# Optimization experiments

Measured on AMD Instinct MI355X. Metric: run time of the kernel, lower is better.

The kernel has to match this reference:

```python
import jax, jax.numpy as jnp
import numpy as np

N_QUBITS = 10
N_LAYERS = 4
DIM = 2 ** N_QUBITS


def _bit(v, q, n):
    return (v >> (n - 1 - q)) & 1


def _cnot_indices(control, target, n):
    idx0, idx1 = [], []
    for i in range(2 ** n):
        if _bit(i, control, n) == 1 and _bit(i, target, n) == 0:
            idx0.append(i)
            idx1.append(i | (1 << (n - 1 - target)))
    return np.asarray(idx0, np.int32), np.asarray(idx1, np.int32)


# static precomputed CNOT swap indices for pairs (q, (q+1) % n)
_CNOT = [_cnot_indices(q, (q + 1) % N_QUBITS, N_QUBITS) for q in range(N_QUBITS)]
# Z expectation masks: [n_qubits, dim] of +/-1
_ZMASK = np.array([[1.0 - 2.0 * _bit(i, q, N_QUBITS) for i in range(DIM)]
                   for q in range(N_QUBITS)], np.float32)


def _rx(t):
    c = jnp.cos(t / 2.0).astype(jnp.complex64)
    s = jnp.sin(t / 2.0).astype(jnp.complex64)
    return jnp.stack([jnp.stack([c, -1j * s], -1),
                      jnp.stack([-1j * s, c], -1)], -2)


def _ry(t):
    c = jnp.cos(t / 2.0).astype(jnp.complex64)
    s = jnp.sin(t / 2.0).astype(jnp.complex64)
    return jnp.stack([jnp.stack([c, -s], -1),
                      jnp.stack([s, c], -1)], -2)


def _rz(t):
    tc = t.astype(jnp.complex64)
    e0 = jnp.exp(-1j * tc / 2.0)
    e1 = jnp.exp(1j * tc / 2.0)
    z = jnp.zeros_like(e0)
    return jnp.stack([jnp.stack([e0, z], -1),
                      jnp.stack([z, e1], -1)], -2)


def _apply_gate(state, gate, q):
    # state: [b, DIM] complex64; gate: [2,2] or [b,2,2]
    b = state.shape[0]
    psi = state.reshape((b,) + (2,) * N_QUBITS)
    psi = jnp.moveaxis(psi, q + 1, N_QUBITS).reshape(b, DIM // 2, 2)
    if gate.ndim == 3:
        out = jnp.einsum('bmi,bij->bmj', psi, gate)
    else:
        out = jnp.einsum('bmi,ij->bmj', psi, gate)
    out = out.reshape((b,) + (2,) * N_QUBITS)
    out = jnp.moveaxis(out, N_QUBITS, q + 1)
    return out.reshape(b, DIM)


def _cnot(state, idx0, idx1):
    return state.at[:, idx0].set(state[:, idx1]).at[:, idx1].set(state[:, idx0])


def setup_inputs() -> dict:
    key = jax.random.key(0)
    k1, k2, k3, k4 = jax.random.split(key, 4)
    x = jax.random.normal(k1, (16384, 3), jnp.float32)
    enc_W = jax.random.normal(k2, (N_QUBITS, 3), jnp.float32) * 0.3
    enc_b = jax.random.normal(k3, (N_QUBITS,), jnp.float32) * 0.1
    theta = jax.random.normal(k4, (N_LAYERS, N_QUBITS, 3), jnp.float32) * 0.04
    return {"x": x, "enc_W": enc_W, "enc_b": enc_b, "theta": theta}


def reference(x, enc_W, enc_b, theta):
    b = x.shape[0]
    enc = jnp.pi * jnp.tanh(x @ enc_W.T + enc_b)  # [b, n_qubits]
    state = jnp.zeros((b, DIM), jnp.complex64).at[:, 0].set(1.0 + 0j)
    # batched encoding RY rotations
    for q in range(N_QUBITS):
        state = _apply_gate(state, _ry(enc[:, q]), q)
    # variational layers (shared gate across batch)
    for layer in range(N_LAYERS):
        for q in range(N_QUBITS):
            state = _apply_gate(state, _rx(theta[layer, q, 0]), q)
            state = _apply_gate(state, _ry(theta[layer, q, 1]), q)
            state = _apply_gate(state, _rz(theta[layer, q, 2]), q)
        for idx0, idx1 in _CNOT:
            state = _cnot(state, idx0, idx1)
    probs = jnp.square(state.real) + jnp.square(state.imag)  # [b, DIM]
    return probs @ jnp.asarray(_ZMASK).T  # [b, n_qubits]
```

## Files before the change

kernel.cpp:

```cpp
#include <hip/hip_runtime.h>
#include <stdint.h>

#define NQ 10
#define NL 4

typedef unsigned int u32;
typedef _Float16 f16x8 __attribute__((ext_vector_type(8)));
typedef float f32x16 __attribute__((ext_vector_type(16)));
typedef u32 u32x4 __attribute__((ext_vector_type(4)));

constexpr u32 FRc(u32 r) {
    u32 r0 = r & 1, r1 = (r >> 1) & 1, r2 = (r >> 2) & 1, r3 = (r >> 3) & 1, r4 = (r >> 4) & 1;
    return (r4 << 9) | ((r3 ^ r4) << 8) | ((r2 ^ r3) << 7) | ((r1 ^ r2) << 6) |
           ((r0 ^ r1) << 5) | (r0 << 4);
}
constexpr u32 FCc(u32 c) {
    u32 c0 = c & 1, c1 = (c >> 1) & 1, c2 = (c >> 2) & 1, c3 = (c >> 3) & 1, c4 = (c >> 4) & 1;
    return (c0 << 9) | (c0 << 8) | (c4 << 4) | ((c3 ^ c4) << 3) | ((c2 ^ c3) << 2) |
           ((c1 ^ c2) << 1) | (c0 ^ c1);
}

__device__ __forceinline__ f32x16 mfma16(f16x8 a, f16x8 b, f32x16 c) {
    return __builtin_amdgcn_mfma_f32_32x32x16_f16(a, b, c, 0, 0, 0);
}
__device__ __forceinline__ f32x16 zero16() {
    f32x16 z;
#pragma unroll
    for (int i = 0; i < 16; i++) z[i] = 0.f;
    return z;
}
__device__ __forceinline__ f16x8 negf(f16x8 v) {
    u32x4 u = __builtin_bit_cast(u32x4, v);
#pragma unroll
    for (int i = 0; i < 4; i++) u[i] ^= 0x80008000u;
    return __builtin_bit_cast(f16x8, u);
}
__device__ __forceinline__ u32 pk2(float a, float b) {
    auto h = __builtin_amdgcn_cvt_pkrtz(a, b);
    return __builtin_bit_cast(u32, h);
}
__device__ __forceinline__ u32 permlo(u32 a, u32 b) { return __builtin_amdgcn_perm(b, a, 0x05040100u); }
__device__ __forceinline__ u32 permhi(u32 a, u32 b) { return __builtin_amdgcn_perm(b, a, 0x07060302u); }
__device__ __forceinline__ f16x8 mk8(u32 a, u32 b, u32 c, u32 d) {
    u32x4 v; v[0] = a; v[1] = b; v[2] = c; v[3] = d;
    return __builtin_bit_cast(f16x8, v);
}
template <int MASK>
__device__ __forceinline__ float swz(float v) {
    return __int_as_float(__builtin_amdgcn_ds_swizzle(__float_as_int(v), (MASK << 10) | 0x1F));
}
__device__ __forceinline__ u32 bpermu(int addr, u32 v) {
    return (u32)__builtin_amdgcn_ds_bpermute(addr, (int)v);
}
__device__ __forceinline__ void cmulh(float ar, float ai, float br, float bi, float& cr, float& ci) {
    cr = ar * br - ai * bi;
    ci = ar * bi + ai * br;
}

__device__ __forceinline__ void c2a(const f32x16& V, bool hb, int addr32, u32 (&o)[8]) {
    u32 pw[8];
#pragma unroll
    for (int p = 0; p < 8; p++) pw[p] = pk2(V[2 * p], V[2 * p + 1]);
    u32 s0 = hb ? pw[0] : pw[2];
    u32 s1 = hb ? pw[1] : pw[3];
    u32 s2 = hb ? pw[4] : pw[6];
    u32 s3 = hb ? pw[5] : pw[7];
    u32 r0 = bpermu(addr32, s0), r1 = bpermu(addr32, s1);
    u32 r2 = bpermu(addr32, s2), r3 = bpermu(addr32, s3);
    o[0] = hb ? r0 : pw[0]; o[1] = hb ? r1 : pw[1];
    o[2] = hb ? pw[2] : r0; o[3] = hb ? pw[3] : r1;
    o[4] = hb ? r2 : pw[4]; o[5] = hb ? r3 : pw[5];
    o[6] = hb ? pw[6] : r2; o[7] = hb ? pw[7] : r3;
}

__global__ void tq_prep(const float* __restrict__ theta, uint16_t* __restrict__ frag) {
    __shared__ float g[NL * NQ][8];
    int tt = threadIdx.x;
    if (tt < NL * NQ) {
        float hx = 0.5f * theta[tt * 3 + 0];
        float hy = 0.5f * theta[tt * 3 + 1];
        float hz = 0.5f * theta[tt * 3 + 2];
        float cx = cosf(hx), sx = sinf(hx);
        float cy = cosf(hy), sy = sinf(hy);
        float cz = cosf(hz), sz = sinf(hz);
        float m00r = cx * cy, m00i = -sx * sy;
        float m01r = -cx * sy, m01i = -sx * cy;
        float m10r = cx * sy, m10i = -sx * cy;
        float m11r = cx * cy, m11i = sx * sy;
        float g00r, g00i, g01r, g01i, g10r, g10i, g11r, g11i;
        cmulh(m00r, m00i, cz, -sz, g00r, g00i);
        cmulh(m10r, m10i, cz, -sz, g10r, g10i);
        cmulh(m01r, m01i, cz, sz, g01r, g01i);
        cmulh(m11r, m11i, cz, sz, g11r, g11i);
        g[tt][0] = g00r; g[tt][1] = g00i; g[tt][2] = g01r; g[tt][3] = g01i;
        g[tt][4] = g10r; g[tt][5] = g10i; g[tt][6] = g11r; g[tt][7] = g11i;
    }
    __syncthreads();
    int t = blockIdx.x * blockDim.x + tt;
    int lane = t & 63, kh = (t >> 6) & 1, part = (t >> 7) & 1, mat = (t >> 8) & 1, l = t >> 9;
    int mn = lane & 31, hf = (lane >> 5) & 1;
#pragma unroll
    for (int j = 0; j < 8; j++) {
        int k = kh * 16 + hf * 8 + j;
        float pr = 1.f, pi = 0.f;
#pragma unroll
        for (int u = 0; u < 5; u++) {
            int q = mat ? (5 + u) : u;
            int bi_ = (k >> (4 - u)) & 1;
            int bo_ = (mn >> (4 - u)) & 1;
            const float* gg = g[l * NQ + q];
            float er = gg[(bi_ * 2 + bo_) * 2 + 0];
            float ei = gg[(bi_ * 2 + bo_) * 2 + 1];
            float nr, ni;
            cmulh(pr, pi, er, ei, nr, ni);
            pr = nr;
            pi = ni;
        }
        float v = part ? pi : pr;
        _Float16 h = (_Float16)v;
        frag[t * 8 + j] = __builtin_bit_cast(unsigned short, h);
    }
    if (blockIdx.x == 0 && tt < 128) {
        int ln = tt & 63, kh2 = tt >> 6;
        int q = ln & 31, hf2 = (ln >> 5) & 1;
        u32 M = (q == 0) ? 0xFu : (q == 1) ? 0x18u : (q == 2) ? 0x1Cu : (q == 3) ? 0x1Eu : 0x1Fu;
        uint16_t* o = frag + ((32 + kh2) * 64 + ln) * 8;
#pragma unroll
        for (int j = 0; j < 8; j++) {
            int k = kh2 * 16 + hf2 * 8 + j;
            float v = (__builtin_popcount((u32)k & M) & 1) ? -1.f : 1.f;
            _Float16 h = (_Float16)v;
            o[j] = __builtin_bit_cast(unsigned short, h);
        }
    }
}

__global__ __launch_bounds__(256) void tq_main(
    const float* __restrict__ x, const float* __restrict__ encW,
    const float* __restrict__ encb, const uint16_t* __restrict__ frag,
    float* __restrict__ out, int batch) {
    __shared__ u32 smem[4 * 1024];
    int tid = threadIdx.x;
    int wave = (blockIdx.x * blockDim.x + tid) >> 6;
    int lane = tid & 63;
    if (wave >= batch) return;
    u32* slab = smem + (tid >> 6) * 1024;
    const int col = lane & 31;
    const int half_ = lane >> 5;
    const bool hb = half_ != 0;
    const int addr32 = (lane ^ 32) << 2;
    const u32 Fc5 = FCc((u32)col);

    float x0 = x[wave * 3 + 0], x1 = x[wave * 3 + 1], x2 = x[wave * 3 + 2];
    float hc = 1.f, hs = 0.f;
    if (lane < NQ) {
        float tta = 3.14159265358979323846f *
                    tanhf(x0 * encW[lane * 3 + 0] + x1 * encW[lane * 3 + 1] +
                          x2 * encW[lane * 3 + 2] + encb[lane]);
        float h = 0.5f * tta;
        hc = cosf(h);
        hs = sinf(h);
    }
    float fcv[NQ], fsv[NQ];
#pragma unroll
    for (int q = 0; q < NQ; q++) {
        fcv[q] = __shfl(hc, q, 64);
        fsv[q] = __shfl(hs, q, 64);
    }
    float colf = 1.f;
    colf *= ((col >> 4) & 1) ? -fsv[5] : fcv[5];
    colf *= ((col >> 3) & 1) ? -fsv[6] : fcv[6];
    colf *= ((col >> 2) & 1) ? -fsv[7] : fcv[7];
    colf *= ((col >> 1) & 1) ? -fsv[8] : fcv[8];
    colf *= (col & 1) ? -fsv[9] : fcv[9];
    float f1h = half_ ? -fsv[1] : fcv[1];
    float gj[8];
#pragma unroll
    for (int j = 0; j < 8; j++) {
        gj[j] = ((j & 4) ? -fsv[2] : fcv[2]) * ((j & 2) ? -fsv[3] : fcv[3]) *
                ((j & 1) ? -fsv[4] : fcv[4]);
    }
    f16x8 Sr0, Sr1, Si0, Si1;
#pragma unroll
    for (int j = 0; j < 8; j++) {
        Sr0[j] = (_Float16)(fcv[0] * f1h * gj[j] * colf);
        Sr1[j] = (_Float16)(-fsv[0] * f1h * gj[j] * colf);
        Si0[j] = (_Float16)0.f;
        Si1[j] = (_Float16)0.f;
    }

    const f16x8* fr = (const f16x8*)frag;
#define FRAG(f) fr[((f)*64) + lane]

    f32x16 Ur, Ui;
#pragma unroll
    for (int l = 0; l < NL; l++) {
        f16x8 Wr0 = FRAG(8 * l + 0), Wr1 = FRAG(8 * l + 1);
        f16x8 Wi0 = FRAG(8 * l + 2), Wi1 = FRAG(8 * l + 3);
        f16x8 Vr0 = FRAG(8 * l + 4), Vr1 = FRAG(8 * l + 5);
        f16x8 Vi0 = FRAG(8 * l + 6), Vi1 = FRAG(8 * l + 7);

        f32x16 Tr = zero16(), Ti = zero16();
        Tr = mfma16(Sr0, Wr0, Tr);
        Tr = mfma16(Sr1, Wr1, Tr);
        Ti = mfma16(Sr0, Wi0, Ti);
        Ti = mfma16(Sr1, Wi1, Ti);
        if (l > 0) {
            f16x8 nSi0 = negf(Si0), nSi1 = negf(Si1);
            Tr = mfma16(nSi0, Wi0, Tr);
            Tr = mfma16(nSi1, Wi1, Tr);
            Ti = mfma16(Si0, Wr0, Ti);
            Ti = mfma16(Si1, Wr1, Ti);
        }

        u32 oR[8], oI[8];
        c2a(Tr, hb, addr32, oR);
        c2a(Ti, hb, addr32, oI);
        f16x8 TAr0 = mk8(oR[0], oR[1], oR[2], oR[3]);
        f16x8 TAr1 = mk8(oR[4], oR[5], oR[6], oR[7]);
        f16x8 TAi0 = mk8(oI[0], oI[1], oI[2], oI[3]);
        f16x8 TAi1 = mk8(oI[4], oI[5], oI[6], oI[7]);

        Ur = zero16();
        Ui = zero16();
        Ur = mfma16(TAr0, Vr0, Ur);
        Ur = mfma16(TAr1, Vr1, Ur);
        {
            f16x8 nTAi0 = negf(TAi0), nTAi1 = negf(TAi1);
            Ur = mfma16(nTAi0, Vi0, Ur);
            Ur = mfma16(nTAi1, Vi1, Ur);
        }
        Ui = mfma16(TAr0, Vi0, Ui);
        Ui = mfma16(TAr1, Vi1, Ui);
        Ui = mfma16(TAi0, Vr0, Ui);
        Ui = mfma16(TAi1, Vr1, Ui);

        if (l < NL - 1) {
            {
                u32* wb = slab + col + half_ * (4 * 32);
#pragma unroll
                for (int gi = 0; gi < 16; gi++) {
                    int rb = (gi & 3) + 8 * (gi >> 2);
                    wb[rb * 32] = pk2(Ur[gi], Ui[gi]);
                }
            }
            u32 sb[16];
            {
                u32 fh = Fc5 ^ (half_ ? FRc(8) : 0u);
#pragma unroll
                for (int kh = 0; kh < 2; kh++)
#pragma unroll
                    for (int j = 0; j < 8; j++)
                        sb[kh * 8 + j] = slab[FRc(kh * 16 + j) ^ fh];
            }
            Sr0 = mk8(permlo(sb[0], sb[1]), permlo(sb[2], sb[3]),
                      permlo(sb[4], sb[5]), permlo(sb[6], sb[7]));
            Sr1 = mk8(permlo(sb[8], sb[9]), permlo(sb[10], sb[11]),
                      permlo(sb[12], sb[13]), permlo(sb[14], sb[15]));
            Si0 = mk8(permhi(sb[0], sb[1]), permhi(sb[2], sb[3]),
                      permhi(sb[4], sb[5]), permhi(sb[6], sb[7]));
            Si1 = mk8(permhi(sb[8], sb[9]), permhi(sb[10], sb[11]),
                      permhi(sb[12], sb[13]), permhi(sb[14], sb[15]));
        }
    }

    f32x16 P;
#pragma unroll
    for (int gi = 0; gi < 16; gi++) P[gi] = Ur[gi] * Ur[gi] + Ui[gi] * Ui[gi];
    u32 po[8];
    c2a(P, hb, addr32, po);
    f16x8 PB0 = mk8(po[0], po[1], po[2], po[3]);
    f16x8 PB1 = mk8(po[4], po[5], po[6], po[7]);
    f16x8 Srw0 = FRAG(32), Srw1 = FRAG(33);
    f32x16 D = mfma16(Srw0, PB0, mfma16(Srw1, PB1, zero16()));

    u32 b4 = (col >> 4) & 1, b3 = (col >> 3) & 1, b2 = (col >> 2) & 1,
        b1 = (col >> 1) & 1, b0 = col & 1;
    u32 p4 = b4, p43 = p4 ^ b3, p432 = p43 ^ b2, p4321 = p432 ^ b1, pall = p4321 ^ b0;
    u32 sg[6];
    sg[0] = hb ? 0u : pall;
    sg[1] = hb ? p4 : 0u;
    sg[2] = hb ? p43 : 0u;
    sg[3] = hb ? p432 : 0u;
    sg[4] = hb ? 0u : p4321;
    sg[5] = hb ? 0u : pall;
    float red[6];
#pragma unroll
    for (int s = 0; s < 6; s++) {
        float v = __uint_as_float(__float_as_uint(D[s]) ^ (sg[s] << 31));
        v += swz<1>(v);
        v += swz<2>(v);
        v += swz<4>(v);
        v += swz<8>(v);
        v += swz<16>(v);
        red[s] = v;
    }
    int cc = col - ((col >= 4) ? 4 : 0);
    float v = red[0];
    v = (cc == 1) ? red[1] : v;
    v = (cc == 2) ? red[2] : v;
    v = (cc == 3) ? red[3] : v;
    v = (cc == 4) ? red[4] : v;
    v = (cc == 5) ? red[5] : v;
    bool st = hb ? (col >= 4 && col < 8) : (col < 4 || col == 8 || col == 9);
    if (st) out[wave * NQ + col] = v;
}

extern "C" void kernel_launch(void* const* d_in, const int* in_sizes, int n_in,
                              void* d_out, int out_size, void* d_ws, size_t ws_size,
                              hipStream_t stream) {
    const float* x = (const float*)d_in[0];
    const float* encW = (const float*)d_in[1];
    const float* encb = (const float*)d_in[2];
    const float* th = (const float*)d_in[3];
    float* out = (float*)d_out;
    uint16_t* frag = (uint16_t*)d_ws;
    int batch = in_sizes[0] / 3;

    tq_prep<<<2, 1024, 0, stream>>>(th, frag);
    int total_threads = batch * 64;
    tq_main<<<(total_threads + 255) / 256, 256, 0, stream>>>(x, encW, encb, frag, out, batch);
}
```

Before: 102.6 us.

## Replace LDS transpose between layers with cross-lane swizzle and bpermute

Removes the per-wave shared-memory slab used to re-layout the state between variational layers. The accumulator is now rearranged in registers with ds_swizzle and ds_bpermute. The permutation is folded into the precomputed gate fragments by Gray-coding the output index for the non-final layers. It also replaces __shfl broadcasts with readlane. This removes LDS write/read traffic and the LDS allocation per block, at the cost of more VALU selects and cross-lane ops.

```diff
diff --git a/kernel.cpp b/kernel.cpp
--- a/kernel.cpp
+++ b/kernel.cpp
@@ -9,16 +9,6 @@
 typedef float f32x16 __attribute__((ext_vector_type(16)));
 typedef u32 u32x4 __attribute__((ext_vector_type(4)));
 
-constexpr u32 FRc(u32 r) {
-    u32 r0 = r & 1, r1 = (r >> 1) & 1, r2 = (r >> 2) & 1, r3 = (r >> 3) & 1, r4 = (r >> 4) & 1;
-    return (r4 << 9) | ((r3 ^ r4) << 8) | ((r2 ^ r3) << 7) | ((r1 ^ r2) << 6) |
-           ((r0 ^ r1) << 5) | (r0 << 4);
-}
-constexpr u32 FCc(u32 c) {
-    u32 c0 = c & 1, c1 = (c >> 1) & 1, c2 = (c >> 2) & 1, c3 = (c >> 3) & 1, c4 = (c >> 4) & 1;
-    return (c0 << 9) | (c0 << 8) | (c4 << 4) | ((c3 ^ c4) << 3) | ((c2 ^ c3) << 2) |
-           ((c1 ^ c2) << 1) | (c0 ^ c1);
-}
 
 __device__ __forceinline__ f32x16 mfma16(f16x8 a, f16x8 b, f32x16 c) {
     return __builtin_amdgcn_mfma_f32_32x32x16_f16(a, b, c, 0, 0, 0);
@@ -49,8 +39,15 @@
 __device__ __forceinline__ float swz(float v) {
     return __int_as_float(__builtin_amdgcn_ds_swizzle(__float_as_int(v), (MASK << 10) | 0x1F));
 }
+template <int MASK>
+__device__ __forceinline__ u32 swzu(u32 v) {
+    return (u32)__builtin_amdgcn_ds_swizzle((int)v, (MASK << 10) | 0x1F);
+}
 __device__ __forceinline__ u32 bpermu(int addr, u32 v) {
     return (u32)__builtin_amdgcn_ds_bpermute(addr, (int)v);
+}
+__device__ __forceinline__ float rdlane(float v, int l) {
+    return __uint_as_float((u32)__builtin_amdgcn_readlane((int)__float_as_uint(v), l));
 }
 __device__ __forceinline__ void cmulh(float ar, float ai, float br, float bi, float& cr, float& ci) {
     cr = ar * br - ai * bi;
@@ -99,6 +96,7 @@
     int t = blockIdx.x * blockDim.x + tt;
     int lane = t & 63, kh = (t >> 6) & 1, part = (t >> 7) & 1, mat = (t >> 8) & 1, l = t >> 9;
     int mn = lane & 31, hf = (lane >> 5) & 1;
+    int mne = (l < NL - 1) ? ((mn ^ (mn >> 1)) & 31) : mn;
 #pragma unroll
     for (int j = 0; j < 8; j++) {
         int k = kh * 16 + hf * 8 + j;
@@ -107,7 +105,7 @@
         for (int u = 0; u < 5; u++) {
             int q = mat ? (5 + u) : u;
             int bi_ = (k >> (4 - u)) & 1;
-            int bo_ = (mn >> (4 - u)) & 1;
+            int bo_ = (mne >> (4 - u)) & 1;
             const float* gg = g[l * NQ + q];
             float er = gg[(bi_ * 2 + bo_) * 2 + 0];
             float ei = gg[(bi_ * 2 + bo_) * 2 + 1];
@@ -139,17 +137,15 @@
     const float* __restrict__ x, const float* __restrict__ encW,
     const float* __restrict__ encb, const uint16_t* __restrict__ frag,
     float* __restrict__ out, int batch) {
-    __shared__ u32 smem[4 * 1024];
     int tid = threadIdx.x;
     int wave = (blockIdx.x * blockDim.x + tid) >> 6;
     int lane = tid & 63;
     if (wave >= batch) return;
-    u32* slab = smem + (tid >> 6) * 1024;
     const int col = lane & 31;
     const int half_ = lane >> 5;
     const bool hb = half_ != 0;
+    const bool c0 = (lane & 1) != 0;
     const int addr32 = (lane ^ 32) << 2;
-    const u32 Fc5 = FCc((u32)col);
 
     float x0 = x[wave * 3 + 0], x1 = x[wave * 3 + 1], x2 = x[wave * 3 + 2];
     float hc = 1.f, hs = 0.f;
@@ -164,8 +160,8 @@
     float fcv[NQ], fsv[NQ];
 #pragma unroll
     for (int q = 0; q < NQ; q++) {
-        fcv[q] = __shfl(hc, q, 64);
-        fsv[q] = __shfl(hs, q, 64);
+        fcv[q] = rdlane(hc, q);
+        fsv[q] = rdlane(hs, q);
     }
     float colf = 1.f;
     colf *= ((col >> 4) & 1) ? -fsv[5] : fcv[5];
@@ -236,31 +232,44 @@
         Ui = mfma16(TAi1, Vr1, Ui);
 
         if (l < NL - 1) {
-            {
-                u32* wb = slab + col + half_ * (4 * 32);
-#pragma unroll
-                for (int gi = 0; gi < 16; gi++) {
-                    int rb = (gi & 3) + 8 * (gi >> 2);
-                    wb[rb * 32] = pk2(Ur[gi], Ui[gi]);
-                }
+            u32 w_[16];
+#pragma unroll
+            for (int gi = 0; gi < 16; gi++) w_[gi] = pk2(Ur[gi], Ui[gi]);
+            u32 sw_[16];
+#pragma unroll
+            for (int gi = 1; gi < 16; gi += 2) sw_[gi] = swzu<0x1F>(w_[gi]);
+            u32 xw[16];
+#pragma unroll
+            for (int gi = 0; gi < 16; gi += 2) xw[gi] = c0 ? w_[gi ^ 8] : w_[gi];
+#pragma unroll
+            for (int gi = 1; gi < 16; gi += 2) xw[gi] = c0 ? sw_[gi ^ 8] : sw_[gi];
+            u32 r_[8];
+#pragma unroll
+            for (int j = 0; j < 4; j++) {
+                u32 s_ = hb ? xw[j] : xw[4 + j];
+                r_[j] = bpermu(addr32, s_);
             }
-            u32 sb[16];
-            {
-                u32 fh = Fc5 ^ (half_ ? FRc(8) : 0u);
-#pragma unroll
-                for (int kh = 0; kh < 2; kh++)
-#pragma unroll
-                    for (int j = 0; j < 8; j++)
-                        sb[kh * 8 + j] = slab[FRc(kh * 16 + j) ^ fh];
+#pragma unroll
+            for (int j = 0; j < 4; j++) {
+                u32 s_ = hb ? xw[8 + j] : xw[12 + j];
+                r_[4 + j] = bpermu(addr32, s_);
             }
-            Sr0 = mk8(permlo(sb[0], sb[1]), permlo(sb[2], sb[3]),
-                      permlo(sb[4], sb[5]), permlo(sb[6], sb[7]));
-            Sr1 = mk8(permlo(sb[8], sb[9]), permlo(sb[10], sb[11]),
-                      permlo(sb[12], sb[13]), permlo(sb[14], sb[15]));
-            Si0 = mk8(permhi(sb[0], sb[1]), permhi(sb[2], sb[3]),
-                      permhi(sb[4], sb[5]), permhi(sb[6], sb[7]));
-            Si1 = mk8(permhi(sb[8], sb[9]), permhi(sb[10], sb[11]),
-                      permhi(sb[12], sb[13]), permhi(sb[14], sb[15]));
+            u32 k0[8], k1[8];
+#pragma unroll
+            for (int t = 0; t < 4; t++) {
+                k0[t] = hb ? r_[t] : xw[t];
+                k0[4 + t] = hb ? xw[4 + t] : r_[t];
+                k1[t] = hb ? r_[4 + t] : xw[8 + t];
+                k1[4 + t] = hb ? xw[12 + t] : r_[4 + t];
+            }
+            Sr0 = mk8(permlo(k0[0], k0[1]), permlo(k0[2], k0[3]),
+                      permlo(k0[4], k0[5]), permlo(k0[6], k0[7]));
+            Sr1 = mk8(permlo(k1[0], k1[1]), permlo(k1[2], k1[3]),
+                      permlo(k1[4], k1[5]), permlo(k1[6], k1[7]));
+            Si0 = mk8(permhi(k0[0], k0[1]), permhi(k0[2], k0[3]),
+                      permhi(k0[4], k0[5]), permhi(k0[6], k0[7]));
+            Si1 = mk8(permhi(k1[0], k1[1]), permhi(k1[2], k1[3]),
+                      permhi(k1[4], k1[5]), permhi(k1[6], k1[7]));
         }
     }
 
```

New measurement: 144.6 us. +40.9%, slower.

## Replace LDS transpose between layers with swizzle/bpermute register shuffles

Applied to the files above, without the earlier changes.

The inter-layer state relayout previously wrote the MFMA accumulator to a per-wave LDS slab and read it back in a CNOT-permuted order. The change folds the row permutation into the precomputed gate fragments (a Gray-code remap of output indices for non-final layers) and performs the remaining transpose with ds_swizzle and ds_bpermute cross-lane exchanges. This removes the shared-memory allocation and the 16 stores plus 16 scattered loads per layer. In exchange it adds select logic and cross-lane ops, and correctness depends on the fragment remap matching the new register layout exactly.

```diff
diff --git a/kernel.cpp b/kernel.cpp
--- a/kernel.cpp
+++ b/kernel.cpp
@@ -9,16 +9,6 @@
 typedef float f32x16 __attribute__((ext_vector_type(16)));
 typedef u32 u32x4 __attribute__((ext_vector_type(4)));
 
-constexpr u32 FRc(u32 r) {
-    u32 r0 = r & 1, r1 = (r >> 1) & 1, r2 = (r >> 2) & 1, r3 = (r >> 3) & 1, r4 = (r >> 4) & 1;
-    return (r4 << 9) | ((r3 ^ r4) << 8) | ((r2 ^ r3) << 7) | ((r1 ^ r2) << 6) |
-           ((r0 ^ r1) << 5) | (r0 << 4);
-}
-constexpr u32 FCc(u32 c) {
-    u32 c0 = c & 1, c1 = (c >> 1) & 1, c2 = (c >> 2) & 1, c3 = (c >> 3) & 1, c4 = (c >> 4) & 1;
-    return (c0 << 9) | (c0 << 8) | (c4 << 4) | ((c3 ^ c4) << 3) | ((c2 ^ c3) << 2) |
-           ((c1 ^ c2) << 1) | (c0 ^ c1);
-}
 
 __device__ __forceinline__ f32x16 mfma16(f16x8 a, f16x8 b, f32x16 c) {
     return __builtin_amdgcn_mfma_f32_32x32x16_f16(a, b, c, 0, 0, 0);
@@ -48,6 +38,10 @@
 template <int MASK>
 __device__ __forceinline__ float swz(float v) {
     return __int_as_float(__builtin_amdgcn_ds_swizzle(__float_as_int(v), (MASK << 10) | 0x1F));
+}
+template <int MASK>
+__device__ __forceinline__ u32 swzu(u32 v) {
+    return (u32)__builtin_amdgcn_ds_swizzle((int)v, (MASK << 10) | 0x1F);
 }
 __device__ __forceinline__ u32 bpermu(int addr, u32 v) {
     return (u32)__builtin_amdgcn_ds_bpermute(addr, (int)v);
@@ -99,6 +93,7 @@
     int t = blockIdx.x * blockDim.x + tt;
     int lane = t & 63, kh = (t >> 6) & 1, part = (t >> 7) & 1, mat = (t >> 8) & 1, l = t >> 9;
     int mn = lane & 31, hf = (lane >> 5) & 1;
+    int mne = (l < NL - 1) ? ((mn ^ (mn >> 1)) & 31) : mn;
 #pragma unroll
     for (int j = 0; j < 8; j++) {
         int k = kh * 16 + hf * 8 + j;
@@ -107,7 +102,7 @@
         for (int u = 0; u < 5; u++) {
             int q = mat ? (5 + u) : u;
             int bi_ = (k >> (4 - u)) & 1;
-            int bo_ = (mn >> (4 - u)) & 1;
+            int bo_ = (mne >> (4 - u)) & 1;
             const float* gg = g[l * NQ + q];
             float er = gg[(bi_ * 2 + bo_) * 2 + 0];
             float ei = gg[(bi_ * 2 + bo_) * 2 + 1];
@@ -139,17 +134,15 @@
     const float* __restrict__ x, const float* __restrict__ encW,
     const float* __restrict__ encb, const uint16_t* __restrict__ frag,
     float* __restrict__ out, int batch) {
-    __shared__ u32 smem[4 * 1024];
     int tid = threadIdx.x;
     int wave = (blockIdx.x * blockDim.x + tid) >> 6;
     int lane = tid & 63;
     if (wave >= batch) return;
-    u32* slab = smem + (tid >> 6) * 1024;
     const int col = lane & 31;
     const int half_ = lane >> 5;
     const bool hb = half_ != 0;
+    const bool c0 = (lane & 1) != 0;
     const int addr32 = (lane ^ 32) << 2;
-    const u32 Fc5 = FCc((u32)col);
 
     float x0 = x[wave * 3 + 0], x1 = x[wave * 3 + 1], x2 = x[wave * 3 + 2];
     float hc = 1.f, hs = 0.f;
@@ -236,31 +229,47 @@
         Ui = mfma16(TAi1, Vr1, Ui);
 
         if (l < NL - 1) {
-            {
-                u32* wb = slab + col + half_ * (4 * 32);
-#pragma unroll
-                for (int gi = 0; gi < 16; gi++) {
-                    int rb = (gi & 3) + 8 * (gi >> 2);
-                    wb[rb * 32] = pk2(Ur[gi], Ui[gi]);
+            u32 srw0[4], srw1[4], siw0[4], siw1[4];
+#pragma unroll
+            for (int pp = 0; pp < 2; pp++) {
+                u32 ka0, ka1, ka4, ka5, kb0, kb1, kb4, kb5;
+#pragma unroll
+                for (int u = 0; u < 2; u++) {
+                    const int t = pp * 2 + u;
+                    u32 wa = pk2(Ur[t], Ui[t]);
+                    u32 wb = pk2(Ur[4 + t], Ui[4 + t]);
+                    u32 wc = pk2(Ur[8 + t], Ui[8 + t]);
+                    u32 wd = pk2(Ur[12 + t], Ui[12 + t]);
+                    u32 xa, xb, xc, xd;
+                    if ((t & 1) == 0) {
+                        xa = c0 ? wc : wa;
+                        xb = c0 ? wd : wb;
+                        xc = c0 ? wa : wc;
+                        xd = c0 ? wb : wd;
+                    } else {
+                        xa = swzu<0x1F>(c0 ? wa : wc);
+                        xb = swzu<0x1F>(c0 ? wb : wd);
+                        xc = swzu<0x1F>(c0 ? wc : wa);
+                        xd = swzu<0x1F>(c0 ? wd : wb);
+                    }
+                    u32 ra = bpermu(addr32, hb ? xa : xb);
+                    u32 rb2 = bpermu(addr32, hb ? xc : xd);
+                    u32 v0 = hb ? ra : xa;
+                    u32 v4 = hb ? xb : ra;
+                    u32 w0 = hb ? rb2 : xc;
+                    u32 w4 = hb ? xd : rb2;
+                    if (u == 0) { ka0 = v0; ka4 = v4; kb0 = w0; kb4 = w4; }
+                    else        { ka1 = v0; ka5 = v4; kb1 = w0; kb5 = w4; }
                 }
+                srw0[pp] = permlo(ka0, ka1); srw0[2 + pp] = permlo(ka4, ka5);
+                srw1[pp] = permlo(kb0, kb1); srw1[2 + pp] = permlo(kb4, kb5);
+                siw0[pp] = permhi(ka0, ka1); siw0[2 + pp] = permhi(ka4, ka5);
+                siw1[pp] = permhi(kb0, kb1); siw1[2 + pp] = permhi(kb4, kb5);
             }
-            u32 sb[16];
-            {
-                u32 fh = Fc5 ^ (half_ ? FRc(8) : 0u);
-#pragma unroll
-                for (int kh = 0; kh < 2; kh++)
-#pragma unroll
-                    for (int j = 0; j < 8; j++)
-                        sb[kh * 8 + j] = slab[FRc(kh * 16 + j) ^ fh];
-            }
-            Sr0 = mk8(permlo(sb[0], sb[1]), permlo(sb[2], sb[3]),
-                      permlo(sb[4], sb[5]), permlo(sb[6], sb[7]));
-            Sr1 = mk8(permlo(sb[8], sb[9]), permlo(sb[10], sb[11]),
-                      permlo(sb[12], sb[13]), permlo(sb[14], sb[15]));
-            Si0 = mk8(permhi(sb[0], sb[1]), permhi(sb[2], sb[3]),
-                      permhi(sb[4], sb[5]), permhi(sb[6], sb[7]));
-            Si1 = mk8(permhi(sb[8], sb[9]), permhi(sb[10], sb[11]),
-                      permhi(sb[12], sb[13]), permhi(sb[14], sb[15]));
+            Sr0 = mk8(srw0[0], srw0[1], srw0[2], srw0[3]);
+            Sr1 = mk8(srw1[0], srw1[1], srw1[2], srw1[3]);
+            Si0 = mk8(siw0[0], siw0[1], siw0[2], siw0[3]);
+            Si1 = mk8(siw1[0], siw1[1], siw1[2], siw1[3]);
         }
     }
 
```

Result: no change. 102.2 us (-0.4%).

## Remap fragment K ordering to drop LDS round-trip and bpermute conversions

Applied to the files above, without the earlier changes.

Reorders the K index mapping of the precomputed gate fragments and folds a Gray-code-like permutation of the output index into the layer matrices. The MFMA accumulator layout can then feed the next MFMA's A operand directly after packing to f16, with no cross-half bpermute. The per-layer LDS write/read of the state is replaced by register selects and a ds_swizzle exchange between neighbouring lanes. This removes shared memory use and LDS traffic per layer, at the cost of a more intricate index mapping that must stay consistent with the CNOT permutation and the initial-state layout.

```diff
diff --git a/kernel.cpp b/kernel.cpp
--- a/kernel.cpp
+++ b/kernel.cpp
@@ -9,16 +9,6 @@
 typedef float f32x16 __attribute__((ext_vector_type(16)));
 typedef u32 u32x4 __attribute__((ext_vector_type(4)));
 
-constexpr u32 FRc(u32 r) {
-    u32 r0 = r & 1, r1 = (r >> 1) & 1, r2 = (r >> 2) & 1, r3 = (r >> 3) & 1, r4 = (r >> 4) & 1;
-    return (r4 << 9) | ((r3 ^ r4) << 8) | ((r2 ^ r3) << 7) | ((r1 ^ r2) << 6) |
-           ((r0 ^ r1) << 5) | (r0 << 4);
-}
-constexpr u32 FCc(u32 c) {
-    u32 c0 = c & 1, c1 = (c >> 1) & 1, c2 = (c >> 2) & 1, c3 = (c >> 3) & 1, c4 = (c >> 4) & 1;
-    return (c0 << 9) | (c0 << 8) | (c4 << 4) | ((c3 ^ c4) << 3) | ((c2 ^ c3) << 2) |
-           ((c1 ^ c2) << 1) | (c0 ^ c1);
-}
 
 __device__ __forceinline__ f32x16 mfma16(f16x8 a, f16x8 b, f32x16 c) {
     return __builtin_amdgcn_mfma_f32_32x32x16_f16(a, b, c, 0, 0, 0);
@@ -39,8 +29,9 @@
     auto h = __builtin_amdgcn_cvt_pkrtz(a, b);
     return __builtin_bit_cast(u32, h);
 }
-__device__ __forceinline__ u32 permlo(u32 a, u32 b) { return __builtin_amdgcn_perm(b, a, 0x05040100u); }
-__device__ __forceinline__ u32 permhi(u32 a, u32 b) { return __builtin_amdgcn_perm(b, a, 0x07060302u); }
+__device__ __forceinline__ u32 mixhl(u32 s, u32 x) {
+    return __builtin_amdgcn_perm(s, x, 0x07060100u);
+}
 __device__ __forceinline__ f16x8 mk8(u32 a, u32 b, u32 c, u32 d) {
     u32x4 v; v[0] = a; v[1] = b; v[2] = c; v[3] = d;
     return __builtin_bit_cast(f16x8, v);
@@ -49,28 +40,13 @@
 __device__ __forceinline__ float swz(float v) {
     return __int_as_float(__builtin_amdgcn_ds_swizzle(__float_as_int(v), (MASK << 10) | 0x1F));
 }
-__device__ __forceinline__ u32 bpermu(int addr, u32 v) {
-    return (u32)__builtin_amdgcn_ds_bpermute(addr, (int)v);
+template <int MASK>
+__device__ __forceinline__ u32 swzu(u32 v) {
+    return (u32)__builtin_amdgcn_ds_swizzle((int)v, (MASK << 10) | 0x1F);
 }
 __device__ __forceinline__ void cmulh(float ar, float ai, float br, float bi, float& cr, float& ci) {
     cr = ar * br - ai * bi;
     ci = ar * bi + ai * br;
-}
-
-__device__ __forceinline__ void c2a(const f32x16& V, bool hb, int addr32, u32 (&o)[8]) {
-    u32 pw[8];
-#pragma unroll
-    for (int p = 0; p < 8; p++) pw[p] = pk2(V[2 * p], V[2 * p + 1]);
-    u32 s0 = hb ? pw[0] : pw[2];
-    u32 s1 = hb ? pw[1] : pw[3];
-    u32 s2 = hb ? pw[4] : pw[6];
-    u32 s3 = hb ? pw[5] : pw[7];
-    u32 r0 = bpermu(addr32, s0), r1 = bpermu(addr32, s1);
-    u32 r2 = bpermu(addr32, s2), r3 = bpermu(addr32, s3);
-    o[0] = hb ? r0 : pw[0]; o[1] = hb ? r1 : pw[1];
-    o[2] = hb ? pw[2] : r0; o[3] = hb ? pw[3] : r1;
-    o[4] = hb ? r2 : pw[4]; o[5] = hb ? r3 : pw[5];
-    o[6] = hb ? pw[6] : r2; o[7] = hb ? pw[7] : r3;
 }
 
 __global__ void tq_prep(const float* __restrict__ theta, uint16_t* __restrict__ frag) {
@@ -99,15 +75,16 @@
     int t = blockIdx.x * blockDim.x + tt;
     int lane = t & 63, kh = (t >> 6) & 1, part = (t >> 7) & 1, mat = (t >> 8) & 1, l = t >> 9;
     int mn = lane & 31, hf = (lane >> 5) & 1;
+    int mne = (l < NL - 1) ? ((mn ^ (mn >> 1)) & 31) : mn;
 #pragma unroll
     for (int j = 0; j < 8; j++) {
-        int k = kh * 16 + hf * 8 + j;
+        int k = kh * 16 + ((j >> 2)) * 8 + hf * 4 + (j & 3);
         float pr = 1.f, pi = 0.f;
 #pragma unroll
         for (int u = 0; u < 5; u++) {
             int q = mat ? (5 + u) : u;
             int bi_ = (k >> (4 - u)) & 1;
-            int bo_ = (mn >> (4 - u)) & 1;
+            int bo_ = (mne >> (4 - u)) & 1;
             const float* gg = g[l * NQ + q];
             float er = gg[(bi_ * 2 + bo_) * 2 + 0];
             float ei = gg[(bi_ * 2 + bo_) * 2 + 1];
@@ -127,7 +104,7 @@
         uint16_t* o = frag + ((32 + kh2) * 64 + ln) * 8;
 #pragma unroll
         for (int j = 0; j < 8; j++) {
-            int k = kh2 * 16 + hf2 * 8 + j;
+            int k = kh2 * 16 + ((j >> 2)) * 8 + hf2 * 4 + (j & 3);
             float v = (__builtin_popcount((u32)k & M) & 1) ? -1.f : 1.f;
             _Float16 h = (_Float16)v;
             o[j] = __builtin_bit_cast(unsigned short, h);
@@ -139,17 +116,14 @@
     const float* __restrict__ x, const float* __restrict__ encW,
     const float* __restrict__ encb, const uint16_t* __restrict__ frag,
     float* __restrict__ out, int batch) {
-    __shared__ u32 smem[4 * 1024];
     int tid = threadIdx.x;
     int wave = (blockIdx.x * blockDim.x + tid) >> 6;
     int lane = tid & 63;
     if (wave >= batch) return;
-    u32* slab = smem + (tid >> 6) * 1024;
     const int col = lane & 31;
     const int half_ = lane >> 5;
     const bool hb = half_ != 0;
-    const int addr32 = (lane ^ 32) << 2;
-    const u32 Fc5 = FCc((u32)col);
+    const bool c0 = (lane & 1) != 0;
 
     float x0 = x[wave * 3 + 0], x1 = x[wave * 3 + 1], x2 = x[wave * 3 + 2];
     float hc = 1.f, hs = 0.f;
@@ -173,18 +147,18 @@
     colf *= ((col >> 2) & 1) ? -fsv[7] : fcv[7];
     colf *= ((col >> 1) & 1) ? -fsv[8] : fcv[8];
     colf *= (col & 1) ? -fsv[9] : fcv[9];
-    float f1h = half_ ? -fsv[1] : fcv[1];
+    float f2h = half_ ? -fsv[2] : fcv[2];
     float gj[8];
 #pragma unroll
     for (int j = 0; j < 8; j++) {
-        gj[j] = ((j & 4) ? -fsv[2] : fcv[2]) * ((j & 2) ? -fsv[3] : fcv[3]) *
+        gj[j] = ((j & 4) ? -fsv[1] : fcv[1]) * ((j & 2) ? -fsv[3] : fcv[3]) *
                 ((j & 1) ? -fsv[4] : fcv[4]);
     }
     f16x8 Sr0, Sr1, Si0, Si1;
 #pragma unroll
     for (int j = 0; j < 8; j++) {
-        Sr0[j] = (_Float16)(fcv[0] * f1h * gj[j] * colf);
-        Sr1[j] = (_Float16)(-fsv[0] * f1h * gj[j] * colf);
+        Sr0[j] = (_Float16)(fcv[0] * f2h * gj[j] * colf);
+        Sr1[j] = (_Float16)(-fsv[0] * f2h * gj[j] * colf);
         Si0[j] = (_Float16)0.f;
         Si1[j] = (_Float16)0.f;
     }
@@ -213,13 +187,21 @@
             Ti = mfma16(Si1, Wr1, Ti);
         }
 
-        u32 oR[8], oI[8];
-        c2a(Tr, hb, addr32, oR);
-        c2a(Ti, hb, addr32, oI);
-        f16x8 TAr0 = mk8(oR[0], oR[1], oR[2], oR[3]);
-        f16x8 TAr1 = mk8(oR[4], oR[5], oR[6], oR[7]);
-        f16x8 TAi0 = mk8(oI[0], oI[1], oI[2], oI[3]);
-        f16x8 TAi1 = mk8(oI[4], oI[5], oI[6], oI[7]);
+        f16x8 TAr0, TAr1, TAi0, TAi1;
+        {
+            u32 a0[4], a1[4], b0[4], b1[4];
+#pragma unroll
+            for (int p = 0; p < 4; p++) {
+                a0[p] = pk2(Tr[2 * p], Tr[2 * p + 1]);
+                a1[p] = pk2(Tr[8 + 2 * p], Tr[8 + 2 * p + 1]);
+                b0[p] = pk2(Ti[2 * p], Ti[2 * p + 1]);
+                b1[p] = pk2(Ti[8 + 2 * p], Ti[8 + 2 * p + 1]);
+            }
+            TAr0 = mk8(a0[0], a0[1], a0[2], a0[3]);
+            TAr1 = mk8(a1[0], a1[1], a1[2], a1[3]);
+            TAi0 = mk8(b0[0], b0[1], b0[2], b0[3]);
+            TAi1 = mk8(b1[0], b1[1], b1[2], b1[3]);
+        }
 
         Ur = zero16();
         Ui = zero16();
@@ -236,41 +218,47 @@
         Ui = mfma16(TAi1, Vr1, Ui);
 
         if (l < NL - 1) {
-            {
-                u32* wb = slab + col + half_ * (4 * 32);
-#pragma unroll
-                for (int gi = 0; gi < 16; gi++) {
-                    int rb = (gi & 3) + 8 * (gi >> 2);
-                    wb[rb * 32] = pk2(Ur[gi], Ui[gi]);
-                }
+            u32 wr0[4], wr1[4], wi0[4], wi1[4];
+#pragma unroll
+            for (int p = 0; p < 4; p++) {
+                wr0[p] = pk2(Ur[2 * p], Ur[2 * p + 1]);
+                wr1[p] = pk2(Ur[8 + 2 * p], Ur[8 + 2 * p + 1]);
+                wi0[p] = pk2(Ui[2 * p], Ui[2 * p + 1]);
+                wi1[p] = pk2(Ui[8 + 2 * p], Ui[8 + 2 * p + 1]);
             }
-            u32 sb[16];
-            {
-                u32 fh = Fc5 ^ (half_ ? FRc(8) : 0u);
-#pragma unroll
-                for (int kh = 0; kh < 2; kh++)
-#pragma unroll
-                    for (int j = 0; j < 8; j++)
-                        sb[kh * 8 + j] = slab[FRc(kh * 16 + j) ^ fh];
+            u32 s0[4], s1[4], t0[4], t1[4];
+#pragma unroll
+            for (int p = 0; p < 4; p++) {
+                u32 xe0r = c0 ? wr1[p] : wr0[p];
+                u32 xe1r = c0 ? wr0[p] : wr1[p];
+                u32 xe0i = c0 ? wi1[p] : wi0[p];
+                u32 xe1i = c0 ? wi0[p] : wi1[p];
+                s0[p] = mixhl(swzu<0x1F>(xe1r), xe0r);
+                s1[p] = mixhl(swzu<0x1F>(xe0r), xe1r);
+                t0[p] = mixhl(swzu<0x1F>(xe1i), xe0i);
+                t1[p] = mixhl(swzu<0x1F>(xe0i), xe1i);
             }
-            Sr0 = mk8(permlo(sb[0], sb[1]), permlo(sb[2], sb[3]),
-                      permlo(sb[4], sb[5]), permlo(sb[6], sb[7]));
-            Sr1 = mk8(permlo(sb[8], sb[9]), permlo(sb[10], sb[11]),
-                      permlo(sb[12], sb[13]), permlo(sb[14], sb[15]));
-            Si0 = mk8(permhi(sb[0], sb[1]), permhi(sb[2], sb[3]),
-                      permhi(sb[4], sb[5]), permhi(sb[6], sb[7]));
-            Si1 = mk8(permhi(sb[8], sb[9]), permhi(sb[10], sb[11]),
-                      permhi(sb[12], sb[13]), permhi(sb[14], sb[15]));
+            Sr0 = mk8(s0[0], s0[1], s0[2], s0[3]);
+            Sr1 = mk8(s1[0], s1[1], s1[2], s1[3]);
+            Si0 = mk8(t0[0], t0[1], t0[2], t0[3]);
+            Si1 = mk8(t1[0], t1[1], t1[2], t1[3]);
         }
     }
 
     f32x16 P;
 #pragma unroll
     for (int gi = 0; gi < 16; gi++) P[gi] = Ur[gi] * Ur[gi] + Ui[gi] * Ui[gi];
-    u32 po[8];
-    c2a(P, hb, addr32, po);
-    f16x8 PB0 = mk8(po[0], po[1], po[2], po[3]);
-    f16x8 PB1 = mk8(po[4], po[5], po[6], po[7]);
+    f16x8 PB0, PB1;
+    {
+        u32 p0[4], p1[4];
+#pragma unroll
+        for (int p = 0; p < 4; p++) {
+            p0[p] = pk2(P[2 * p], P[2 * p + 1]);
+            p1[p] = pk2(P[8 + 2 * p], P[8 + 2 * p + 1]);
+        }
+        PB0 = mk8(p0[0], p0[1], p0[2], p0[3]);
+        PB1 = mk8(p1[0], p1[1], p1[2], p1[3]);
+    }
     f16x8 Srw0 = FRAG(32), Srw1 = FRAG(33);
     f32x16 D = mfma16(Srw0, PB0, mfma16(Srw1, PB1, zero16()));
 
```

Result: faster. 98.09 us (-4.4%).
